# Performance work log

Measured on AMD Instinct MI355X. Metric: run time of the kernel, lower is better.

Reference implementation:

```python
import jax, jax.numpy as jnp
import numpy as np

NUM_HEAD = 16
HEAD_DIM = 64
RES_DIM = 1024
LN_EPS = 1e-5


def setup_inputs() -> dict:
    key = jax.random.key(0)
    k1, k2, k3 = jax.random.split(key, 3)
    slen, bsz = 2048, 4
    x = jax.random.normal(k1, (slen, bsz, RES_DIM), dtype=jnp.float32)
    # torch Linear weights: [out_features, in_features]
    w_qkv = jax.random.normal(k2, (NUM_HEAD * 3 * HEAD_DIM, RES_DIM), dtype=jnp.float32) * (1.0 / np.sqrt(RES_DIM))
    w_out = jax.random.normal(k3, (RES_DIM, NUM_HEAD * HEAD_DIM), dtype=jnp.float32) * (1.0 / np.sqrt(NUM_HEAD * HEAD_DIM))
    ln_w = jnp.ones((RES_DIM,), dtype=jnp.float32)
    ln_b = jnp.zeros((RES_DIM,), dtype=jnp.float32)
    return {"x": x, "w_qkv": w_qkv, "w_out": w_out, "ln_w": ln_w, "ln_b": ln_b}


def _layer_norm(x, w, b):
    mu = jnp.mean(x, axis=-1, keepdims=True)
    var = jnp.var(x, axis=-1, keepdims=True)
    return (x - mu) * jax.lax.rsqrt(var + LN_EPS) * w + b


def reference(x, w_qkv, w_out, ln_w, ln_b):
    slen, bsz, _ = x.shape
    scale = 1.0 / np.sqrt(RES_DIM).astype(np.float32)  # note: res_dim, not head_dim
    x_in = _layer_norm(x, ln_w, ln_b)  # pre_lnorm=True
    qkv = x_in @ w_qkv.T  # [s, b, n*3*d]
    qkv = qkv.reshape(slen, bsz, NUM_HEAD, 3 * HEAD_DIM)
    q, k, v = jnp.split(qkv, 3, axis=-1)  # each [s, b, n, d]
    scores = jnp.einsum('ibnd,jbnd->ijbn', q, k) * scale
    attn = jax.nn.softmax(scores, axis=1)  # softmax over keys j
    attn_out = jnp.einsum('ijbn,jbnd->ibnd', attn, v)
    attn_out = attn_out.reshape(slen, bsz, NUM_HEAD * HEAD_DIM)
    attn_out = attn_out @ w_out.T
    return x + attn_out
```

## Files before the change

kernel.cpp:

```cpp
#include <hip/hip_runtime.h>

typedef __bf16 bf16_t;
typedef __bf16 bf16x2 __attribute__((ext_vector_type(2)));
typedef __bf16 bf16x4 __attribute__((ext_vector_type(4)));
typedef __bf16 bf16x8 __attribute__((ext_vector_type(8)));
typedef float f32x4 __attribute__((ext_vector_type(4)));

#define S_LEN 2048
#define BSZ 4
#define NHEAD 16
#define HDIM 64
#define RDIM 1024
#define QKV_N 3072
#define NTOK 8192

__device__ static inline void gload_lds16(const void* g, void* l) {
    __builtin_amdgcn_global_load_lds(
        (const __attribute__((address_space(1))) void*)(unsigned long long)g,
        (__attribute__((address_space(3))) void*)(unsigned long long)l,
        16, 0, 0);
}

__global__ __launch_bounds__(256) void ln_kernel(const float* __restrict__ x,
                                                 const float* __restrict__ lw,
                                                 const float* __restrict__ lb,
                                                 bf16_t* __restrict__ xn) {
    int row = blockIdx.x;
    int tid = threadIdx.x;
    const float4* xr = (const float4*)(x + (size_t)row * RDIM);
    float4 v = xr[tid];
    float s  = v.x + v.y + v.z + v.w;
    float ss = v.x*v.x + v.y*v.y + v.z*v.z + v.w*v.w;
#pragma unroll
    for (int off = 1; off < 64; off <<= 1) {
        s  += __shfl_xor(s, off, 64);
        ss += __shfl_xor(ss, off, 64);
    }
    __shared__ float red[8];
    int wid = tid >> 6, lane = tid & 63;
    if (lane == 0) { red[wid] = s; red[wid + 4] = ss; }
    __syncthreads();
    float S  = red[0] + red[1] + red[2] + red[3];
    float SS = red[4] + red[5] + red[6] + red[7];
    float mu  = S * (1.f / RDIM);
    float var = SS * (1.f / RDIM) - mu * mu;
    float rsig = rsqrtf(var + 1e-5f);
    float4 wv = ((const float4*)lw)[tid];
    float4 bv = ((const float4*)lb)[tid];
    bf16x4 o;
    o[0] = (bf16_t)((v.x - mu) * rsig * wv.x + bv.x);
    o[1] = (bf16_t)((v.y - mu) * rsig * wv.y + bv.y);
    o[2] = (bf16_t)((v.z - mu) * rsig * wv.z + bv.z);
    o[3] = (bf16_t)((v.w - mu) * rsig * wv.w + bv.w);
    *(bf16x4*)(xn + (size_t)row * RDIM + tid * 4) = o;
}

__global__ __launch_bounds__(256) void cvt_kernel(const float* __restrict__ src,
                                                  bf16_t* __restrict__ dst, int n4) {
    int i = blockIdx.x * 256 + threadIdx.x;
    if (i < n4) {
        float4 v = ((const float4*)src)[i];
        bf16x4 o;
        o[0] = (bf16_t)v.x; o[1] = (bf16_t)v.y; o[2] = (bf16_t)v.z; o[3] = (bf16_t)v.w;
        ((bf16x4*)dst)[i] = o;
    }
}

template <int MODE>
__global__ __launch_bounds__(256) void gemm_bt_kernel(const bf16_t* __restrict__ A,
                                                      const bf16_t* __restrict__ Bm,
                                                      bf16_t* __restrict__ Cb,
                                                      const float* __restrict__ X,
                                                      float* __restrict__ Cf,
                                                      int ldc) {
    const int K = 1024;
    __shared__ bf16_t As[128 * 32];
    __shared__ bf16_t Bs[128 * 32];
    int tid = threadIdx.x;
    int lane = tid & 63, wid = tid >> 6;
    int l15 = lane & 15, lg = lane >> 4;
    int wm = wid >> 1, wn = wid & 1;
    int row0 = blockIdx.y * 128;
    int col0 = blockIdx.x * 128;

    int sr = tid >> 2;
    int sc = (tid & 3) * 8;
    const bf16_t* aSrc = A + (size_t)(row0 + sr) * K + sc;
    const bf16_t* bSrc = Bm + (size_t)(col0 + sr) * K + sc;
    bf16_t* aDst = As + tid * 8;
    bf16_t* bDst = Bs + tid * 8;

    f32x4 acc[4][4] = {};
    for (int kt = 0; kt < K; kt += 32) {
        gload_lds16(aSrc + kt, aDst);
        gload_lds16(aSrc + kt + (size_t)64 * K, aDst + 2048);
        gload_lds16(bSrc + kt, bDst);
        gload_lds16(bSrc + kt + (size_t)64 * K, bDst + 2048);
        __syncthreads();
        bf16x8 a[4], b[4];
#pragma unroll
        for (int m = 0; m < 4; m++)
            a[m] = *(const bf16x8*)(As + (wm * 64 + m * 16 + l15) * 32 + lg * 8);
#pragma unroll
        for (int n = 0; n < 4; n++)
            b[n] = *(const bf16x8*)(Bs + (wn * 64 + n * 16 + l15) * 32 + lg * 8);
#pragma unroll
        for (int m = 0; m < 4; m++)
#pragma unroll
            for (int n = 0; n < 4; n++)
                acc[m][n] = __builtin_amdgcn_mfma_f32_16x16x32_bf16(a[m], b[n], acc[m][n], 0, 0, 0);
        __syncthreads();
    }

    int crow = row0 + wm * 64 + lg * 4;
    int ccol = col0 + wn * 64 + l15;
#pragma unroll
    for (int m = 0; m < 4; m++) {
#pragma unroll
        for (int n = 0; n < 4; n++) {
#pragma unroll
            for (int r = 0; r < 4; r++) {
                int rr = crow + m * 16 + r;
                int cc = ccol + n * 16;
                size_t idx = (size_t)rr * ldc + cc;
                if (MODE == 0) {
                    Cb[idx] = (bf16_t)acc[m][n][r];
                } else {
                    Cf[idx] = acc[m][n][r] + X[idx];
                }
            }
        }
    }
}

__global__ __launch_bounds__(256) void attn_kernel(const bf16_t* __restrict__ qkv,
                                                   bf16_t* __restrict__ aout) {
    __shared__ bf16_t Ks[64 * 72];
    __shared__ bf16_t VTs[64 * 72];
    __shared__ bf16_t Ps[4][16 * 72];
    int tid = threadIdx.x;
    int lane = tid & 63, wid = tid >> 6;
    int l15 = lane & 15, lg = lane >> 4;
    int b = blockIdx.y, h = blockIdx.z;
    int sq = blockIdx.x * 64 + wid * 16 + l15;

    const bf16_t* qbase = qkv + (size_t)(sq * 4 + b) * QKV_N + h * 192;
    bf16x8 qf0 = *(const bf16x8*)(qbase + lg * 8);
    bf16x8 qf1 = *(const bf16x8*)(qbase + 32 + lg * 8);

    float mrun = -3e38f, lrun = 0.f;
    f32x4 o[4] = {};
    const float scale = 0.03125f;

    int krow = tid >> 2;
    int kcol = (tid & 3) * 16;
    int vr0 = (tid & 31) * 2;
    int vc0 = (tid >> 5) * 8;

    for (int kv0 = 0; kv0 < S_LEN; kv0 += 64) {
        __syncthreads();
        {
            const bf16_t* ksrc = qkv + (size_t)((kv0 + krow) * 4 + b) * QKV_N + h * 192 + 64 + kcol;
            bf16x8 k0 = *(const bf16x8*)ksrc;
            bf16x8 k1 = *(const bf16x8*)(ksrc + 8);
            const bf16_t* vsrc = qkv + (size_t)((kv0 + vr0) * 4 + b) * QKV_N + h * 192 + 128 + vc0;
            bf16x8 v0 = *(const bf16x8*)vsrc;
            bf16x8 v1 = *(const bf16x8*)(vsrc + 4 * QKV_N);
            *(bf16x8*)(Ks + krow * 72 + kcol) = k0;
            *(bf16x8*)(Ks + krow * 72 + kcol + 8) = k1;
#pragma unroll
            for (int i = 0; i < 8; i++) {
                bf16x2 pr; pr[0] = v0[i]; pr[1] = v1[i];
                *(bf16x2*)(VTs + (vc0 + i) * 72 + vr0) = pr;
            }
        }
        __syncthreads();

        f32x4 sc4[4];
#pragma unroll
        for (int kb = 0; kb < 4; kb++) {
            bf16x8 ka = *(const bf16x8*)(Ks + (kb * 16 + l15) * 72 + lg * 8);
            bf16x8 kc = *(const bf16x8*)(Ks + (kb * 16 + l15) * 72 + 32 + lg * 8);
            f32x4 z = {0.f, 0.f, 0.f, 0.f};
            z = __builtin_amdgcn_mfma_f32_16x16x32_bf16(ka, qf0, z, 0, 0, 0);
            z = __builtin_amdgcn_mfma_f32_16x16x32_bf16(kc, qf1, z, 0, 0, 0);
            sc4[kb] = z;
        }

        float tmax = -3e38f;
#pragma unroll
        for (int kb = 0; kb < 4; kb++)
#pragma unroll
            for (int r = 0; r < 4; r++) tmax = fmaxf(tmax, sc4[kb][r]);
        tmax = fmaxf(tmax, __shfl_xor(tmax, 16, 64));
        tmax = fmaxf(tmax, __shfl_xor(tmax, 32, 64));
        float mnew = fmaxf(mrun, tmax * scale);
        float corr = __expf(mrun - mnew);
        float lsum = 0.f;
#pragma unroll
        for (int kb = 0; kb < 4; kb++) {
            float p0 = __expf(sc4[kb][0] * scale - mnew);
            float p1 = __expf(sc4[kb][1] * scale - mnew);
            float p2 = __expf(sc4[kb][2] * scale - mnew);
            float p3 = __expf(sc4[kb][3] * scale - mnew);
            lsum += (p0 + p1) + (p2 + p3);
            bf16x2 q01; q01[0] = (bf16_t)p0; q01[1] = (bf16_t)p1;
            bf16x2 q23; q23[0] = (bf16_t)p2; q23[1] = (bf16_t)p3;
            *(bf16x2*)(&Ps[wid][l15 * 72 + kb * 16 + lg * 4]) = q01;
            *(bf16x2*)(&Ps[wid][l15 * 72 + kb * 16 + lg * 4 + 2]) = q23;
        }
        lsum += __shfl_xor(lsum, 16, 64);
        lsum += __shfl_xor(lsum, 32, 64);
        lrun = lrun * corr + lsum;
        mrun = mnew;
#pragma unroll
        for (int dc = 0; dc < 4; dc++) {
            o[dc][0] *= corr; o[dc][1] *= corr; o[dc][2] *= corr; o[dc][3] *= corr;
        }

#pragma unroll
        for (int kc = 0; kc < 2; kc++) {
            bf16x8 pf = *(const bf16x8*)(&Ps[wid][l15 * 72 + kc * 32 + lg * 8]);
#pragma unroll
            for (int dc = 0; dc < 4; dc++) {
                bf16x8 vf = *(const bf16x8*)(VTs + (dc * 16 + l15) * 72 + kc * 32 + lg * 8);
                o[dc] = __builtin_amdgcn_mfma_f32_16x16x32_bf16(vf, pf, o[dc], 0, 0, 0);
            }
        }
    }

    float linv = 1.f / lrun;
    bf16_t* ob = aout + (size_t)(sq * 4 + b) * RDIM + h * 64 + lg * 4;
#pragma unroll
    for (int dc = 0; dc < 4; dc++) {
        bf16x4 ov;
        ov[0] = (bf16_t)(o[dc][0] * linv);
        ov[1] = (bf16_t)(o[dc][1] * linv);
        ov[2] = (bf16_t)(o[dc][2] * linv);
        ov[3] = (bf16_t)(o[dc][3] * linv);
        *(bf16x4*)(ob + dc * 16) = ov;
    }
}

extern "C" void kernel_launch(void* const* d_in, const int* in_sizes, int n_in,
                              void* d_out, int out_size, void* d_ws, size_t ws_size,
                              hipStream_t stream) {
    (void)in_sizes; (void)n_in; (void)out_size; (void)ws_size;
    const float* x     = (const float*)d_in[0];
    const float* w_qkv = (const float*)d_in[1];
    const float* w_out = (const float*)d_in[2];
    const float* ln_w  = (const float*)d_in[3];
    const float* ln_b  = (const float*)d_in[4];
    float* out = (float*)d_out;
    char* ws = (char*)d_ws;

    bf16_t* xn      = (bf16_t*)(ws);
    bf16_t* wqkv_bf = (bf16_t*)(ws + 16777216);
    bf16_t* wout_bf = (bf16_t*)(ws + 23068672);
    bf16_t* qkvb    = (bf16_t*)(ws + 25165824);
    bf16_t* attn    = xn;

    ln_kernel<<<NTOK, 256, 0, stream>>>(x, ln_w, ln_b, xn);
    cvt_kernel<<<3072, 256, 0, stream>>>(w_qkv, wqkv_bf, (QKV_N * RDIM) / 4);
    cvt_kernel<<<1024, 256, 0, stream>>>(w_out, wout_bf, (RDIM * RDIM) / 4);

    gemm_bt_kernel<0><<<dim3(QKV_N / 128, NTOK / 128), 256, 0, stream>>>(
        xn, wqkv_bf, qkvb, nullptr, nullptr, QKV_N);

    attn_kernel<<<dim3(S_LEN / 64, BSZ, NHEAD), 256, 0, stream>>>(qkvb, attn);

    gemm_bt_kernel<1><<<dim3(RDIM / 128, NTOK / 128), 256, 0, stream>>>(
        attn, wout_bf, nullptr, x, out, RDIM);
}
```

Baseline: 348.5 us.

## Double-buffer K/V tiles in attention with async global-to-LDS K loads and swizzle

```diff
diff --git a/kernel.cpp b/kernel.cpp
--- a/kernel.cpp
+++ b/kernel.cpp
@@ -135,59 +135,83 @@
 
 __global__ __launch_bounds__(256) void attn_kernel(const bf16_t* __restrict__ qkv,
                                                    bf16_t* __restrict__ aout) {
-    __shared__ bf16_t Ks[64 * 72];
-    __shared__ bf16_t VTs[64 * 72];
-    __shared__ bf16_t Ps[4][16 * 72];
+    __shared__ __align__(16) bf16_t Kb[2][4096];
+    __shared__ __align__(16) bf16_t VTb[2][64 * 72];
+    __shared__ __align__(16) bf16_t Ps[4][16 * 88];
     int tid = threadIdx.x;
     int lane = tid & 63, wid = tid >> 6;
     int l15 = lane & 15, lg = lane >> 4;
     int b = blockIdx.y, h = blockIdx.z;
     int sq = blockIdx.x * 64 + wid * 16 + l15;
 
+    const float scale = 0.03125f;
+
     const bf16_t* qbase = qkv + (size_t)(sq * 4 + b) * QKV_N + h * 192;
     bf16x8 qf0 = *(const bf16x8*)(qbase + lg * 8);
     bf16x8 qf1 = *(const bf16x8*)(qbase + 32 + lg * 8);
 
+    int kKeyOff = lane >> 3;
+    int kChunk  = (lane & 7) ^ (lane >> 3);
+    int vr0 = (tid & 31) * 2;
+    int vc0 = (tid >> 5) * 8;
+
+    int sw = l15 & 7;
+    int koA = ((lg ^ sw)) * 8;
+    int koC = (((lg + 4) ^ sw)) * 8;
+
     float mrun = -3e38f, lrun = 0.f;
     f32x4 o[4] = {};
-    const float scale = 0.03125f;
-
-    int krow = tid >> 2;
-    int kcol = (tid & 3) * 16;
-    int vr0 = (tid & 31) * 2;
-    int vc0 = (tid >> 5) * 8;
-
-    for (int kv0 = 0; kv0 < S_LEN; kv0 += 64) {
-        __syncthreads();
-        {
-            const bf16_t* ksrc = qkv + (size_t)((kv0 + krow) * 4 + b) * QKV_N + h * 192 + 64 + kcol;
-            bf16x8 k0 = *(const bf16x8*)ksrc;
-            bf16x8 k1 = *(const bf16x8*)(ksrc + 8);
-            const bf16_t* vsrc = qkv + (size_t)((kv0 + vr0) * 4 + b) * QKV_N + h * 192 + 128 + vc0;
-            bf16x8 v0 = *(const bf16x8*)vsrc;
-            bf16x8 v1 = *(const bf16x8*)(vsrc + 4 * QKV_N);
-            *(bf16x8*)(Ks + krow * 72 + kcol) = k0;
-            *(bf16x8*)(Ks + krow * 72 + kcol + 8) = k1;
-#pragma unroll
-            for (int i = 0; i < 8; i++) {
-                bf16x2 pr; pr[0] = v0[i]; pr[1] = v1[i];
-                *(bf16x2*)(VTs + (vc0 + i) * 72 + vr0) = pr;
-            }
-        }
-        __syncthreads();
-
+
+    {
+        const bf16_t* ks = qkv + (size_t)(((0 + wid * 16 + kKeyOff) * 4 + b)) * QKV_N + h * 192 + 64 + kChunk * 8;
+        bf16_t* kd = &Kb[0][wid * 1024 + lane * 8];
+        gload_lds16(ks, kd);
+        gload_lds16(ks + (size_t)8 * 4 * QKV_N, kd + 512);
+        const bf16_t* vs = qkv + (size_t)((0 + vr0) * 4 + b) * QKV_N + h * 192 + 128 + vc0;
+        bf16x8 v0 = *(const bf16x8*)vs;
+        bf16x8 v1 = *(const bf16x8*)(vs + (size_t)4 * QKV_N);
+#pragma unroll
+        for (int i = 0; i < 8; i++) {
+            bf16x2 pr; pr[0] = v0[i]; pr[1] = v1[i];
+            *(bf16x2*)(&VTb[0][(vc0 + i) * 72 + vr0]) = pr;
+        }
+    }
+    __syncthreads();
+
+    int cur = 0;
+    for (int t = 0; t < S_LEN / 64; t++) {
+        bf16x8 v0, v1;
+        bool do_stage = (t + 1) < (S_LEN / 64);
+        if (do_stage) {
+            int kv0 = (t + 1) * 64;
+            const bf16_t* ks = qkv + (size_t)(((kv0 + wid * 16 + kKeyOff) * 4 + b)) * QKV_N + h * 192 + 64 + kChunk * 8;
+            bf16_t* kd = &Kb[cur ^ 1][wid * 1024 + lane * 8];
+            gload_lds16(ks, kd);
+            gload_lds16(ks + (size_t)8 * 4 * QKV_N, kd + 512);
+            const bf16_t* vs = qkv + (size_t)((kv0 + vr0) * 4 + b) * QKV_N + h * 192 + 128 + vc0;
+            v0 = *(const bf16x8*)vs;
+            v1 = *(const bf16x8*)(vs + (size_t)4 * QKV_N);
+        }
+
+        const bf16_t* kbase = &Kb[cur][l15 * 64];
+        bf16x8 kfA[4], kfC[4];
+#pragma unroll
+        for (int kb = 0; kb < 4; kb++) {
+            kfA[kb] = *(const bf16x8*)(kbase + kb * 1024 + koA);
+            kfC[kb] = *(const bf16x8*)(kbase + kb * 1024 + koC);
+        }
         f32x4 sc4[4];
+        __builtin_amdgcn_s_setprio(1);
 #pragma unroll
         for (int kb = 0; kb < 4; kb++) {
-            bf16x8 ka = *(const bf16x8*)(Ks + (kb * 16 + l15) * 72 + lg * 8);
-            bf16x8 kc = *(const bf16x8*)(Ks + (kb * 16 + l15) * 72 + 32 + lg * 8);
             f32x4 z = {0.f, 0.f, 0.f, 0.f};
-            z = __builtin_amdgcn_mfma_f32_16x16x32_bf16(ka, qf0, z, 0, 0, 0);
-            z = __builtin_amdgcn_mfma_f32_16x16x32_bf16(kc, qf1, z, 0, 0, 0);
+            z = __builtin_amdgcn_mfma_f32_16x16x32_bf16(kfA[kb], qf0, z, 0, 0, 0);
+            z = __builtin_amdgcn_mfma_f32_16x16x32_bf16(kfC[kb], qf1, z, 0, 0, 0);
             sc4[kb] = z;
         }
-
-        float tmax = -3e38f;
+        __builtin_amdgcn_s_setprio(0);
+
+        float tmax = sc4[0][0];
 #pragma unroll
         for (int kb = 0; kb < 4; kb++)
 #pragma unroll
@@ -204,10 +228,9 @@
             float p2 = __expf(sc4[kb][2] * scale - mnew);
             float p3 = __expf(sc4[kb][3] * scale - mnew);
             lsum += (p0 + p1) + (p2 + p3);
-            bf16x2 q01; q01[0] = (bf16_t)p0; q01[1] = (bf16_t)p1;
-            bf16x2 q23; q23[0] = (bf16_t)p2; q23[1] = (bf16_t)p3;
-            *(bf16x2*)(&Ps[wid][l15 * 72 + kb * 16 + lg * 4]) = q01;
-            *(bf16x2*)(&Ps[wid][l15 * 72 + kb * 16 + lg * 4 + 2]) = q23;
+            bf16x4 pw;
+            pw[0] = (bf16_t)p0; pw[1] = (bf16_t)p1; pw[2] = (bf16_t)p2; pw[3] = (bf16_t)p3;
+            *(bf16x4*)(&Ps[wid][l15 * 88 + kb * 16 + lg * 4]) = pw;
         }
         lsum += __shfl_xor(lsum, 16, 64);
         lsum += __shfl_xor(lsum, 32, 64);
@@ -218,15 +241,28 @@
             o[dc][0] *= corr; o[dc][1] *= corr; o[dc][2] *= corr; o[dc][3] *= corr;
         }
 
+        if (do_stage) {
+#pragma unroll
+            for (int i = 0; i < 8; i++) {
+                bf16x2 pr; pr[0] = v0[i]; pr[1] = v1[i];
+                *(bf16x2*)(&VTb[cur ^ 1][(vc0 + i) * 72 + vr0]) = pr;
+            }
+        }
+
 #pragma unroll
         for (int kc = 0; kc < 2; kc++) {
-            bf16x8 pf = *(const bf16x8*)(&Ps[wid][l15 * 72 + kc * 32 + lg * 8]);
+            bf16x8 pf = *(const bf16x8*)(&Ps[wid][l15 * 88 + kc * 32 + lg * 8]);
+            __builtin_amdgcn_s_setprio(1);
 #pragma unroll
             for (int dc = 0; dc < 4; dc++) {
-                bf16x8 vf = *(const bf16x8*)(VTs + (dc * 16 + l15) * 72 + kc * 32 + lg * 8);
+                bf16x8 vf = *(const bf16x8*)(&VTb[cur][(dc * 16 + l15) * 72 + kc * 32 + lg * 8]);
                 o[dc] = __builtin_amdgcn_mfma_f32_16x16x32_bf16(vf, pf, o[dc], 0, 0, 0);
             }
-        }
+            __builtin_amdgcn_s_setprio(0);
+        }
+
+        __syncthreads();
+        cur ^= 1;
     }
 
     float linv = 1.f / lrun;
```

Measured after the change: 329.0 us. 5.6% less time.
